# Kernel optimization log

Hardware: AMD Instinct MI355X
Metric: run time of the kernel (lower is better)

Reference implementation:

```python
import jax, jax.numpy as jnp
import numpy as np

N_NODES = 100000
N_EDGES = 1600000
D_FEAT = 128


def setup_inputs() -> dict:
    key = jax.random.key(0)
    k1, k2, k3, k4 = jax.random.split(key, 4)
    support = jax.random.normal(k1, (N_NODES, D_FEAT), dtype=jnp.float32)
    vals = jax.random.uniform(k2, (N_EDGES,), dtype=jnp.float32)
    rows = jax.random.randint(k3, (N_EDGES,), 0, N_NODES, dtype=jnp.int64)
    cols = jax.random.randint(k4, (N_EDGES,), 0, N_NODES, dtype=jnp.int64)
    return {"support": support, "vals": vals, "rows": rows, "cols": cols}


def reference(support, vals, rows, cols):
    # out = adj @ support, adj given in COO: adj[rows[e], cols[e]] = vals[e]
    # Gather neighbor features, scale by edge weight, scatter-add to row nodes.
    msgs = vals[:, None] * support[cols]          # [E, F]
    out = jax.ops.segment_sum(msgs, rows, num_segments=support.shape[0])  # [N, F]
    return out
```

## Files before the change

### kernel.cpp

```cpp
#include <hip/hip_runtime.h>
#include <hip/hip_bf16.h>
#include <hip/hip_fp16.h>


#define D_FEAT 128
#define F4 32
#define H4 32
#define H8 16
#define STRIDE 64
#define CELL 32
#define OVF_CAP 131072
#define EPT 8
#define GMAXIT 13
#define MAXSLOT 3840
#define BROWS 200
#define GT 512

typedef float    vfloat4 __attribute__((ext_vector_type(4)));
typedef _Float16 half4v  __attribute__((ext_vector_type(4)));
typedef _Float16 half8v  __attribute__((ext_vector_type(8)));


__global__ __launch_bounds__(1024) void
phase1_bin_kernel(const float4* __restrict__ support4,
                  half8v* __restrict__ supporth,
                  const int* __restrict__ rows,
                  const int* __restrict__ cols,
                  const float* __restrict__ vals,
                  int2* __restrict__ coarse,
                  int* __restrict__ cellcnt,
                  int4* __restrict__ ovf,
                  int* __restrict__ ovf_count,
                  int E, int BT, int NBLK, int ND, int n8) {
    int b = blockIdx.x;
    int tid = threadIdx.x;

    if (b >= NBLK) {
        int m = (b - NBLK) * 1024 + tid;
        if (m < n8) {
            float4 a0 = support4[(size_t)m * 2];
            float4 a1 = support4[(size_t)m * 2 + 1];
            half8v h;
            h[0] = (_Float16)a0.x; h[1] = (_Float16)a0.y;
            h[2] = (_Float16)a0.z; h[3] = (_Float16)a0.w;
            h[4] = (_Float16)a1.x; h[5] = (_Float16)a1.y;
            h[6] = (_Float16)a1.z; h[7] = (_Float16)a1.w;
            supporth[m] = h;
        }
        return;
    }

    __shared__ int  hist[512];
    __shared__ int  off[513];
    __shared__ int2 sorted[1024 * EPT];

    for (int i = tid; i < 512; i += 1024) hist[i] = 0;
    __syncthreads();

    int t = b * 1024 + tid;
    int   r[EPT];
    int   c[EPT];
    float v[EPT];
    int   rk[EPT];

    #pragma unroll
    for (int i = 0; i < EPT; ++i) {
        int e = t + i * BT;
        r[i] = (e < E) ? rows[e] : -1;
    }
    #pragma unroll
    for (int i = 0; i < EPT; ++i) {
        int e = t + i * BT;
        if (e < E) { c[i] = cols[e]; v[i] = vals[e]; }
    }
    #pragma unroll
    for (int i = 0; i < EPT; ++i)
        rk[i] = (r[i] >= 0) ? atomicAdd(&hist[r[i] / BROWS], 1) : 0;
    __syncthreads();

    if (tid < 64) {
        int l[8];
        int s = 0;
        #pragma unroll
        for (int k = 0; k < 8; ++k) {
            int hv = hist[tid * 8 + k];
            l[k] = (hv < CELL) ? hv : CELL;
            s += l[k];
        }
        int inc = s;
        #pragma unroll
        for (int dd = 1; dd < 64; dd <<= 1) {
            int tt = __shfl_up(inc, dd, 64);
            if (tid >= dd) inc += tt;
        }
        int run = inc - s;
        #pragma unroll
        for (int k = 0; k < 8; ++k) {
            off[tid * 8 + k] = run;
            run += l[k];
        }
        if (tid == 63) off[512] = run;
    }
    __syncthreads();

    #pragma unroll
    for (int i = 0; i < EPT; ++i) {
        if (r[i] < 0) continue;
        int d = r[i] / BROWS;
        if (rk[i] < CELL) {
            int2 q;
            q.x = ((r[i] - d * BROWS) << 17) | c[i];
            q.y = __float_as_int(v[i]);
            sorted[off[d] + rk[i]] = q;
        } else {
            int o = atomicAdd(ovf_count, 1);
            if (o < OVF_CAP) {
                int4 q;
                q.x = r[i]; q.y = c[i]; q.z = __float_as_int(v[i]); q.w = 0;
                ovf[o] = q;
            }
        }
    }
    __syncthreads();

    {
        int grp  = tid >> 4;
        int lane = tid & 15;
        for (int d = grp; d < 512; d += 64) {
            int o = off[d];
            int l = off[d + 1] - o;
            size_t gbase = ((size_t)d * NBLK + b) * CELL;
            for (int k = lane; k < l; k += 16)
                coarse[gbase + k] = sorted[o + k];
        }
    }
    for (int d = tid; d < ND; d += 1024) {
        int h = hist[d];
        cellcnt[(size_t)d * NBLK + b] = (h < CELL) ? h : CELL;
    }
}


__global__ __launch_bounds__(GT) void
bucket_csr_gather_kernel(const half8v* __restrict__ supporth,
                         const int2* __restrict__ coarse,
                         const int* __restrict__ cellcnt,
                         float4* __restrict__ out4,
                         int NBLK, int N) {
    __shared__ int  cnt[257];
    __shared__ int  off[257];
    __shared__ int  ccl[256];
    __shared__ int2 csr[MAXSLOT + 8];

    const int d   = blockIdx.x;
    const int tid = threadIdx.x;
    const int2* cbase = coarse + (size_t)d * NBLK * CELL;
    const int total = NBLK * CELL;

    if (tid < 257) cnt[tid] = 0;
    for (int i = tid; i < NBLK; i += GT)
        ccl[i] = cellcnt[(size_t)d * NBLK + i];
    __syncthreads();

    int2 ent[GMAXIT];
    int  err[GMAXIT];
    int  ernk[GMAXIT];
    #pragma unroll
    for (int it = 0; it < GMAXIT; ++it) {
        int s = tid + it * GT;
        err[it] = -1;
        if (s < total && (s & (CELL - 1)) < ccl[s >> 5]) {
            int2 q = cbase[s];
            int r = (q.x >> 17) & 255;
            ent[it].x = q.x & 0x1FFFF;
            ent[it].y = q.y;
            err[it] = r;
            ernk[it] = atomicAdd(&cnt[r], 1);
        }
    }
    __syncthreads();

    if (tid < 64) {
        int4 c4 = ((int4*)cnt)[tid];
        int t0 = c4.x;
        int t1 = t0 + c4.y;
        int t2 = t1 + c4.z;
        int t3 = t2 + c4.w;
        int inc = t3;
        #pragma unroll
        for (int dd = 1; dd < 64; dd <<= 1) {
            int t = __shfl_up(inc, dd, 64);
            if (tid >= dd) inc += t;
        }
        int excl = inc - t3;
        off[tid * 4 + 0] = excl;
        off[tid * 4 + 1] = excl + t0;
        off[tid * 4 + 2] = excl + t1;
        off[tid * 4 + 3] = excl + t2;
        if (tid == 63) off[256] = inc;
    }
    __syncthreads();

    #pragma unroll
    for (int it = 0; it < GMAXIT; ++it) {
        if (err[it] >= 0) {
            int idx = off[err[it]] + ernk[it];
            if (idx < MAXSLOT + 8) csr[idx] = ent[it];
        }
    }
    __syncthreads();

    const int g = tid >> 4;
    const int i = tid & 15;
    const int base = d * BROWS;
    for (int rq = 0; rq < 7; ++rq) {
        int r = rq * 32 + g;
        if (r >= BROWS) continue;
        int beg = off[r];
        int end = off[r + 1];
        vfloat4 a00 = {0.f,0.f,0.f,0.f}, a01 = {0.f,0.f,0.f,0.f};
        vfloat4 a10 = {0.f,0.f,0.f,0.f}, a11 = {0.f,0.f,0.f,0.f};
        for (int k0 = beg; k0 < end; k0 += 8) {
            int   cc[8];
            float vv[8];
            #pragma unroll
            for (int u = 0; u < 8; ++u) {
                int2 e = csr[k0 + u];
                bool ib = (k0 + u) < end;
                cc[u] = ib ? e.x : 0;
                vv[u] = ib ? __int_as_float(e.y) : 0.f;
            }
            half8v s[8];
            #pragma unroll
            for (int u = 0; u < 8; ++u)
                s[u] = supporth[(size_t)cc[u] * H8 + i];
            #pragma unroll
            for (int u = 0; u < 8; ++u) {
                float v = vv[u];
                if (u & 1) {
                    a10.x += v * (float)s[u][0];
                    a10.y += v * (float)s[u][1];
                    a10.z += v * (float)s[u][2];
                    a10.w += v * (float)s[u][3];
                    a11.x += v * (float)s[u][4];
                    a11.y += v * (float)s[u][5];
                    a11.z += v * (float)s[u][6];
                    a11.w += v * (float)s[u][7];
                } else {
                    a00.x += v * (float)s[u][0];
                    a00.y += v * (float)s[u][1];
                    a00.z += v * (float)s[u][2];
                    a00.w += v * (float)s[u][3];
                    a01.x += v * (float)s[u][4];
                    a01.y += v * (float)s[u][5];
                    a01.z += v * (float)s[u][6];
                    a01.w += v * (float)s[u][7];
                }
            }
        }
        int row = base + r;
        if (row < N) {
            vfloat4 r0, r1;
            r0.x = a00.x + a10.x; r0.y = a00.y + a10.y;
            r0.z = a00.z + a10.z; r0.w = a00.w + a10.w;
            r1.x = a01.x + a11.x; r1.y = a01.y + a11.y;
            r1.z = a01.z + a11.z; r1.w = a01.w + a11.w;
            float4* dst = &out4[(size_t)row * F4 + (i << 1)];
            __builtin_nontemporal_store(r0, (vfloat4*)dst);
            __builtin_nontemporal_store(r1, (vfloat4*)(dst + 1));
        }
    }
}


__global__ void ovf_scatter_kernel(const float* __restrict__ support,
                                   const int4* __restrict__ ovf,
                                   const int* __restrict__ ovf_count,
                                   float* __restrict__ out, int cap) {
    int gid = blockIdx.x * blockDim.x + threadIdx.x;
    int i = gid >> 5;
    int j = gid & 31;
    int istride = (gridDim.x * blockDim.x) >> 5;
    int cnt = *ovf_count;
    if (cnt > cap) cnt = cap;
    for (; i < cnt; i += istride) {
        int4 q = ovf[i];
        float v = __int_as_float(q.z);
        const float4* s4 = (const float4*)support + (size_t)q.y * F4 + j;
        float4 s = *s4;
        float* o = out + (size_t)q.x * D_FEAT + j * 4;
        unsafeAtomicAdd(o + 0, v * s.x);
        unsafeAtomicAdd(o + 1, v * s.y);
        unsafeAtomicAdd(o + 2, v * s.z);
        unsafeAtomicAdd(o + 3, v * s.w);
    }
}


__global__ void convert_kernel(const float4* __restrict__ in,
                               half8v* __restrict__ out, int n8) {
    int t = blockIdx.x * blockDim.x + threadIdx.x;
    if (t >= n8) return;
    float4 a = in[(size_t)t * 2];
    float4 b = in[(size_t)t * 2 + 1];
    half8v h;
    h[0] = (_Float16)a.x; h[1] = (_Float16)a.y;
    h[2] = (_Float16)a.z; h[3] = (_Float16)a.w;
    h[4] = (_Float16)b.x; h[5] = (_Float16)b.y;
    h[6] = (_Float16)b.z; h[7] = (_Float16)b.w;
    out[t] = h;
}

__global__ void gather_half_kernel(const half4v* __restrict__ supporth,
                                   const int* __restrict__ cursor,
                                   const int2* __restrict__ pairs,
                                   float4* __restrict__ out4, int n_nodes) {
    unsigned int t = blockIdx.x * blockDim.x + threadIdx.x;
    unsigned int row = t >> 5;
    unsigned int j = t & 31;
    if (row >= (unsigned int)n_nodes) return;
    int deg = cursor[row];
    if (deg > STRIDE) deg = STRIDE;
    const int2* pr = pairs + (size_t)row * STRIDE;
    int2 z = {0, 0};
    int2 p0 = ((int)j < deg) ? pr[j] : z;
    int2 p1 = ((int)(j + 32) < deg) ? pr[j + 32] : z;
    int   c0 = p0.x;  float v0 = __int_as_float(p0.y);
    int   c1 = p1.x;  float v1 = __int_as_float(p1.y);
    int degr = (deg + 7) & ~7;
    float4 acc[4];
    #pragma unroll
    for (int u = 0; u < 4; ++u) acc[u] = {0.f, 0.f, 0.f, 0.f};
    for (int k = 0; k < degr; k += 8) {
        int   cc[8];
        float vv[8];
        #pragma unroll
        for (int u = 0; u < 8; ++u) {
            int kk = k + u;
            cc[u] = __shfl(kk < 32 ? c0 : c1, kk & 31, 32);
            vv[u] = __shfl(kk < 32 ? v0 : v1, kk & 31, 32);
        }
        half4v s[8];
        #pragma unroll
        for (int u = 0; u < 8; ++u)
            s[u] = supporth[(size_t)cc[u] * H4 + j];
        #pragma unroll
        for (int u = 0; u < 8; ++u) {
            acc[u & 3].x += vv[u] * (float)s[u][0];
            acc[u & 3].y += vv[u] * (float)s[u][1];
            acc[u & 3].z += vv[u] * (float)s[u][2];
            acc[u & 3].w += vv[u] * (float)s[u][3];
        }
    }
    vfloat4 res;
    res.x = (acc[0].x + acc[1].x) + (acc[2].x + acc[3].x);
    res.y = (acc[0].y + acc[1].y) + (acc[2].y + acc[3].y);
    res.z = (acc[0].z + acc[1].z) + (acc[2].z + acc[3].z);
    res.w = (acc[0].w + acc[1].w) + (acc[2].w + acc[3].w);
    __builtin_nontemporal_store(res, (vfloat4*)&out4[(size_t)row * F4 + j]);
}

__global__ void bucket_ilp_kernel(const int* __restrict__ rows,
                                  const int* __restrict__ cols,
                                  const float* __restrict__ vals,
                                  int* __restrict__ cursor,
                                  int* __restrict__ ovf_count,
                                  int2* __restrict__ pairs,
                                  int4* __restrict__ ovf,
                                  int n_edges, int gstride) {
    int tid = blockIdx.x * blockDim.x + threadIdx.x;
    int   r[EPT];
    int   c[EPT];
    float v[EPT];
    int   slot[EPT];
    #pragma unroll
    for (int i = 0; i < EPT; ++i) {
        int e = tid + i * gstride;
        r[i] = (e < n_edges) ? rows[e] : -1;
    }
    #pragma unroll
    for (int i = 0; i < EPT; ++i) {
        int e = tid + i * gstride;
        if (e < n_edges) { c[i] = cols[e]; v[i] = vals[e]; }
    }
    #pragma unroll
    for (int i = 0; i < EPT; ++i)
        slot[i] = (r[i] >= 0) ? atomicAdd(&cursor[r[i]], 1) : 0;
    #pragma unroll
    for (int i = 0; i < EPT; ++i) {
        if (r[i] < 0) continue;
        int2 p;
        p.x = c[i];
        p.y = __float_as_int(v[i]);
        if (slot[i] < STRIDE) {
            pairs[(size_t)r[i] * STRIDE + slot[i]] = p;
        } else {
            int o = atomicAdd(ovf_count, 1);
            if (o < OVF_CAP) {
                int4 q; q.x = r[i]; q.y = p.x; q.z = p.y; q.w = 0;
                ovf[o] = q;
            }
        }
    }
}


__global__ void gc_scatter_kernel(const float* __restrict__ support,
                                  const float* __restrict__ vals,
                                  const int* __restrict__ rows,
                                  const int* __restrict__ cols,
                                  float* __restrict__ out, int n_edges) {
    unsigned int t = blockIdx.x * blockDim.x + threadIdx.x;
    unsigned int e = t >> 5;
    unsigned int j = t & 31;
    if (e >= (unsigned int)n_edges) return;
    int r = rows[e];
    int c = cols[e];
    float v = vals[e];
    const float4* s4 = reinterpret_cast<const float4*>(support) + (size_t)c * F4 + j;
    float4 s = *s4;
    float* o = out + (size_t)r * D_FEAT + j * 4;
    unsafeAtomicAdd(o + 0, v * s.x);
    unsafeAtomicAdd(o + 1, v * s.y);
    unsafeAtomicAdd(o + 2, v * s.z);
    unsafeAtomicAdd(o + 3, v * s.w);
}


extern "C" void kernel_launch(void* const* d_in, const int* in_sizes, int n_in,
                              void* d_out, int out_size, void* d_ws, size_t ws_size,
                              hipStream_t stream) {
    const float* support = (const float*)d_in[0];
    const float* vals    = (const float*)d_in[1];
    const int*   rows    = (const int*)d_in[2];
    const int*   cols    = (const int*)d_in[3];
    float* out = (float*)d_out;

    int E = in_sizes[1];
    int N = in_sizes[0] / D_FEAT;
    int n8 = N * D_FEAT / 8;
    int ND = (N + BROWS - 1) / BROWS;
    int NBLK = (E + 1024 * EPT - 1) / (1024 * EPT);
    int BT = NBLK * 1024;

    char* ws = (char*)d_ws;
    size_t cur = 0;
    auto carve = [&](size_t bytes) -> void* {
        void* p = ws + cur;
        cur += (bytes + 255) & ~(size_t)255;
        return p;
    };

    {
        size_t save = cur;
        int2*   coarse    = (int2*)carve((size_t)ND * NBLK * CELL * 8);
        int*    cellcnt   = (int*)carve((size_t)ND * NBLK * 4);
        int4*   ovf       = (int4*)carve((size_t)OVF_CAP * 16);
        int*    ovf_count = (int*)carve(256);
        half8v* supporth  = (half8v*)carve((size_t)N * D_FEAT * 2);
        if (cur <= ws_size && ND <= 512 && NBLK <= 256 && NBLK * CELL <= GT * GMAXIT) {
            (void)hipMemsetAsync(ovf_count, 0, 4, stream);
            int cblocks = (n8 + 1023) / 1024;
            phase1_bin_kernel<<<NBLK + cblocks, 1024, 0, stream>>>(
                (const float4*)support, supporth, rows, cols, vals,
                coarse, cellcnt, ovf, ovf_count, E, BT, NBLK, ND, n8);
            bucket_csr_gather_kernel<<<ND, GT, 0, stream>>>(
                supporth, coarse, cellcnt, (float4*)out, NBLK, N);
            ovf_scatter_kernel<<<128, 256, 0, stream>>>(
                support, ovf, ovf_count, out, OVF_CAP);
            return;
        }
        cur = save;
    }

    {
        size_t save = cur;
        int*    cursor   = (int*)carve((size_t)(N + 1) * 4);
        int2*   pairs    = (int2*)carve((size_t)N * STRIDE * 8);
        int4*   ovf      = (int4*)carve((size_t)8192 * 16);
        half8v* supporth = (half8v*)carve((size_t)N * D_FEAT * 2);
        if (cur <= ws_size) {
            int* ovf_count = cursor + N;
            int bthreads = (E + EPT - 1) / EPT;
            int bblocks = (bthreads + 255) / 256;
            int gstride = bblocks * 256;
            (void)hipMemsetAsync(cursor, 0, (size_t)(N + 1) * 4, stream);
            convert_kernel<<<(n8 + 255) / 256, 256, 0, stream>>>(
                (const float4*)support, supporth, n8);
            bucket_ilp_kernel<<<bblocks, 256, 0, stream>>>(
                rows, cols, vals, cursor, ovf_count, pairs, ovf, E, gstride);
            unsigned int gthreads = (unsigned int)N * 32;
            gather_half_kernel<<<(gthreads + 255) / 256, 256, 0, stream>>>(
                (const half4v*)supporth, cursor, pairs, (float4*)out, N);
            ovf_scatter_kernel<<<512, 256, 0, stream>>>(
                support, ovf, ovf_count, out, 8192);
            return;
        }
        cur = save;
    }

    (void)hipMemsetAsync(d_out, 0, (size_t)out_size * sizeof(float), stream);
    unsigned int total = (unsigned int)E * 32;
    gc_scatter_kernel<<<(total + 255) / 256, 256, 0, stream>>>(
        support, vals, rows, cols, out, E);
}
```

Before: 185.7 us.

## Replace per-block fixed cells with dense per-bucket arrays via global atomic cursors

The binning phase stops writing each block's edges into fixed 32-slot cells per bucket, which were padded and needed a cell-count array. It now reserves a contiguous range in a dense per-bucket array of capacity 4096 with one global atomicAdd per bucket per block. Overflow now happens only when a bucket exceeds its capacity, not when a block's local cell fills. The gather kernel reads a compact, contiguous list with fewer iterations and no per-cell validity checks. Binning blocks shrink to 512 threads, which roughly doubles their number and therefore the global atomic traffic, and output order now depends on atomic order.

```diff
diff --git a/kernel.cpp b/kernel.cpp
--- a/kernel.cpp
+++ b/kernel.cpp
@@ -8,11 +8,11 @@
 #define H4 32
 #define H8 16
 #define STRIDE 64
-#define CELL 32
 #define OVF_CAP 131072
 #define EPT 8
-#define GMAXIT 13
-#define MAXSLOT 3840
+#define BINT 512
+#define CAP 4096
+#define GMAXIT 8
 #define BROWS 200
 #define GT 512
 
@@ -21,22 +21,22 @@
 typedef _Float16 half8v  __attribute__((ext_vector_type(8)));
 
 
-__global__ __launch_bounds__(1024) void
+__global__ __launch_bounds__(BINT) void
 phase1_bin_kernel(const float4* __restrict__ support4,
                   half8v* __restrict__ supporth,
                   const int* __restrict__ rows,
                   const int* __restrict__ cols,
                   const float* __restrict__ vals,
-                  int2* __restrict__ coarse,
-                  int* __restrict__ cellcnt,
+                  int2* __restrict__ dense,
+                  int* __restrict__ gcur,
                   int4* __restrict__ ovf,
                   int* __restrict__ ovf_count,
-                  int E, int BT, int NBLK, int ND, int n8) {
+                  int E, int BT, int NBLK, int n8) {
     int b = blockIdx.x;
     int tid = threadIdx.x;
 
     if (b >= NBLK) {
-        int m = (b - NBLK) * 1024 + tid;
+        int m = (b - NBLK) * BINT + tid;
         if (m < n8) {
             float4 a0 = support4[(size_t)m * 2];
             float4 a1 = support4[(size_t)m * 2 + 1];
@@ -52,12 +52,13 @@
 
     __shared__ int  hist[512];
     __shared__ int  off[513];
-    __shared__ int2 sorted[1024 * EPT];
-
-    for (int i = tid; i < 512; i += 1024) hist[i] = 0;
-    __syncthreads();
-
-    int t = b * 1024 + tid;
+    __shared__ int  sstart[512];
+    __shared__ int2 sorted[BINT * EPT];
+
+    for (int i = tid; i < 512; i += BINT) hist[i] = 0;
+    __syncthreads();
+
+    int t = b * BINT + tid;
     int   r[EPT];
     int   c[EPT];
     float v[EPT];
@@ -83,8 +84,7 @@
         int s = 0;
         #pragma unroll
         for (int k = 0; k < 8; ++k) {
-            int hv = hist[tid * 8 + k];
-            l[k] = (hv < CELL) ? hv : CELL;
+            l[k] = hist[tid * 8 + k];
             s += l[k];
         }
         int inc = s;
@@ -107,59 +107,65 @@
     for (int i = 0; i < EPT; ++i) {
         if (r[i] < 0) continue;
         int d = r[i] / BROWS;
-        if (rk[i] < CELL) {
-            int2 q;
-            q.x = ((r[i] - d * BROWS) << 17) | c[i];
-            q.y = __float_as_int(v[i]);
-            sorted[off[d] + rk[i]] = q;
-        } else {
-            int o = atomicAdd(ovf_count, 1);
-            if (o < OVF_CAP) {
-                int4 q;
-                q.x = r[i]; q.y = c[i]; q.z = __float_as_int(v[i]); q.w = 0;
-                ovf[o] = q;
-            }
-        }
+        int2 q;
+        q.x = ((r[i] - d * BROWS) << 17) | c[i];
+        q.y = __float_as_int(v[i]);
+        sorted[off[d] + rk[i]] = q;
+    }
+    __syncthreads();
+
+    {
+        int l = off[tid + 1] - off[tid];
+        sstart[tid] = (l > 0) ? atomicAdd(&gcur[tid], l) : 0;
     }
     __syncthreads();
 
     {
         int grp  = tid >> 4;
         int lane = tid & 15;
-        for (int d = grp; d < 512; d += 64) {
-            int o = off[d];
-            int l = off[d + 1] - o;
-            size_t gbase = ((size_t)d * NBLK + b) * CELL;
-            for (int k = lane; k < l; k += 16)
-                coarse[gbase + k] = sorted[o + k];
-        }
-    }
-    for (int d = tid; d < ND; d += 1024) {
-        int h = hist[d];
-        cellcnt[(size_t)d * NBLK + b] = (h < CELL) ? h : CELL;
+        for (int d = grp; d < 512; d += 32) {
+            int o  = off[d];
+            int l  = off[d + 1] - o;
+            int st = sstart[d];
+            for (int k = lane; k < l; k += 16) {
+                int pos = st + k;
+                int2 q = sorted[o + k];
+                if (pos < CAP) {
+                    dense[(size_t)d * CAP + pos] = q;
+                } else {
+                    int ox = atomicAdd(ovf_count, 1);
+                    if (ox < OVF_CAP) {
+                        int4 e4;
+                        e4.x = d * BROWS + ((q.x >> 17) & 255);
+                        e4.y = q.x & 0x1FFFF;
+                        e4.z = q.y;
+                        e4.w = 0;
+                        ovf[ox] = e4;
+                    }
+                }
+            }
+        }
     }
 }
 
 
 __global__ __launch_bounds__(GT) void
 bucket_csr_gather_kernel(const half8v* __restrict__ supporth,
-                         const int2* __restrict__ coarse,
-                         const int* __restrict__ cellcnt,
-                         float4* __restrict__ out4,
-                         int NBLK, int N) {
+                         const int2* __restrict__ dense,
+                         const int* __restrict__ gcur,
+                         float4* __restrict__ out4, int N) {
     __shared__ int  cnt[257];
     __shared__ int  off[257];
-    __shared__ int  ccl[256];
-    __shared__ int2 csr[MAXSLOT + 8];
+    __shared__ int2 csr[CAP + 8];
 
     const int d   = blockIdx.x;
     const int tid = threadIdx.x;
-    const int2* cbase = coarse + (size_t)d * NBLK * CELL;
-    const int total = NBLK * CELL;
+    const int2* dbase = dense + (size_t)d * CAP;
+
+    int total = gcur[d];
+    if (total > CAP) total = CAP;
 
     if (tid < 257) cnt[tid] = 0;
-    for (int i = tid; i < NBLK; i += GT)
-        ccl[i] = cellcnt[(size_t)d * NBLK + i];
     __syncthreads();
 
     int2 ent[GMAXIT];
@@ -169,8 +175,8 @@
     for (int it = 0; it < GMAXIT; ++it) {
         int s = tid + it * GT;
         err[it] = -1;
-        if (s < total && (s & (CELL - 1)) < ccl[s >> 5]) {
-            int2 q = cbase[s];
+        if (s < total) {
+            int2 q = dbase[s];
             int r = (q.x >> 17) & 255;
             ent[it].x = q.x & 0x1FFFF;
             ent[it].y = q.y;
@@ -203,10 +209,8 @@
 
     #pragma unroll
     for (int it = 0; it < GMAXIT; ++it) {
-        if (err[it] >= 0) {
-            int idx = off[err[it]] + ernk[it];
-            if (idx < MAXSLOT + 8) csr[idx] = ent[it];
-        }
+        if (err[it] >= 0)
+            csr[off[err[it]] + ernk[it]] = ent[it];
     }
     __syncthreads();
 
@@ -440,8 +444,8 @@
     int N = in_sizes[0] / D_FEAT;
     int n8 = N * D_FEAT / 8;
     int ND = (N + BROWS - 1) / BROWS;
-    int NBLK = (E + 1024 * EPT - 1) / (1024 * EPT);
-    int BT = NBLK * 1024;
+    int NBLK = (E + BINT * EPT - 1) / (BINT * EPT);
+    int BT = NBLK * BINT;
 
     char* ws = (char*)d_ws;
     size_t cur = 0;
@@ -453,19 +457,19 @@
 
     {
         size_t save = cur;
-        int2*   coarse    = (int2*)carve((size_t)ND * NBLK * CELL * 8);
-        int*    cellcnt   = (int*)carve((size_t)ND * NBLK * 4);
+        int2*   dense     = (int2*)carve((size_t)512 * CAP * 8);
+        int*    gcur      = (int*)carve((size_t)768 * 4);
         int4*   ovf       = (int4*)carve((size_t)OVF_CAP * 16);
-        int*    ovf_count = (int*)carve(256);
         half8v* supporth  = (half8v*)carve((size_t)N * D_FEAT * 2);
-        if (cur <= ws_size && ND <= 512 && NBLK <= 256 && NBLK * CELL <= GT * GMAXIT) {
-            (void)hipMemsetAsync(ovf_count, 0, 4, stream);
-            int cblocks = (n8 + 1023) / 1024;
-            phase1_bin_kernel<<<NBLK + cblocks, 1024, 0, stream>>>(
+        if (cur <= ws_size && ND <= 512) {
+            int* ovf_count = gcur + 512;
+            (void)hipMemsetAsync(gcur, 0, (size_t)513 * 4, stream);
+            int cblocks = (n8 + BINT - 1) / BINT;
+            phase1_bin_kernel<<<NBLK + cblocks, BINT, 0, stream>>>(
                 (const float4*)support, supporth, rows, cols, vals,
-                coarse, cellcnt, ovf, ovf_count, E, BT, NBLK, ND, n8);
+                dense, gcur, ovf, ovf_count, E, BT, NBLK, n8);
             bucket_csr_gather_kernel<<<ND, GT, 0, stream>>>(
-                supporth, coarse, cellcnt, (float4*)out, NBLK, N);
+                supporth, dense, gcur, (float4*)out, N);
             ovf_scatter_kernel<<<128, 256, 0, stream>>>(
                 support, ovf, ovf_count, out, OVF_CAP);
             return;
```

Result: no change. 185.0 us (-0.4%).
